# Optimization experiments

Hardware: AMD Instinct MI355X
Metric: run time of the kernel (lower is better)

Reference implementation:

```python
import jax, jax.numpy as jnp
import numpy as np

N, H, LAT, V = 256, 450, 56, 780  # nodes, hidden_size, latent_size, vocab_size


def _build_tree(seed=0):
    """Random tree on N nodes + DFS path matching the torch dfs() (children in ascending id order)."""
    rng = np.random.default_rng(seed)
    children = [[] for _ in range(N)]
    for i in range(1, N):
        children[int(rng.integers(0, i))].append(i)
    path = []
    stack = [(0, 0)]
    while stack:
        u, ci = stack.pop()
        ch = children[u]
        if ci < len(ch):
            stack.append((u, ci + 1))
            path.append((u, 1))   # descend to child -> stop flag 1
            stack.append((ch[ci], 0))
        else:
            path.append((u, 0))   # backtrack -> stop flag 0
    return path


def setup_inputs() -> dict:
    key = jax.random.key(0)
    ks = jax.random.split(key, 18)
    path = _build_tree()
    L = len(path)  # 2N-1 = 511
    node_ids = np.array([p[0] for p in path], dtype=np.int32)
    stops = np.array([p[1] for p in path], dtype=np.int32)
    next_ids = np.concatenate([node_ids[1:], np.zeros(1, np.int32)])
    label_steps = np.where(stops == 1)[0].astype(np.int32)  # N-1 steps that emit a label
    rng = np.random.default_rng(1)
    vids = rng.integers(0, V, size=N).astype(np.int32)
    node_feature = np.zeros((N, V), np.float32)
    node_feature[np.arange(N), vids] = 1.0  # one-hot vocab features, as in JT-VAE
    real_labels = np.concatenate([vids[:1], vids[next_ids[label_steps]]]).astype(np.int32)  # [N]
    w = lambda k, shape: (jax.random.normal(k, shape, jnp.float32) * 0.05)
    return {
        "latent_code": jax.random.normal(ks[0], (LAT,), jnp.float32),
        "node_feature": jnp.asarray(node_feature),
        "node_ids": jnp.asarray(node_ids),
        "next_ids": jnp.asarray(next_ids),
        "stops": jnp.asarray(stops),
        "label_steps": jnp.asarray(label_steps),
        "real_labels": jnp.asarray(real_labels),
        "Wz_w": w(ks[1], (H, V + H)), "Wz_b": w(ks[2], (H,)),
        "Ur_w": w(ks[3], (H, H)),
        "Wr_w": w(ks[4], (H, V)), "Wr_b": w(ks[5], (H,)),
        "Wh_w": w(ks[6], (H, V + H)), "Wh_b": w(ks[7], (H,)),
        "Wd12_w": w(ks[8], (H, V + LAT)), "Wd12_b": w(ks[9], (H,)),
        "Wd3_w": w(ks[10], (H, H)), "Wd3_b": w(ks[11], (H,)),
        "Ud_w": w(ks[12], (1, 2 * H)), "Ud_b": w(ks[13], (1,)),
        "Wl_w": w(ks[14], (H, H + LAT)), "Wl_b": w(ks[15], (H,)),
        "Ul_w": w(ks[16], (V, H)), "Ul_b": w(ks[17], (V,)),
    }


def reference(latent_code, node_feature, node_ids, next_ids, stops, label_steps, real_labels,
              Wz_w, Wz_b, Ur_w, Wr_w, Wr_b, Wh_w, Wh_b, Wd12_w, Wd12_b, Wd3_w, Wd3_b,
              Ud_w, Ud_b, Wl_w, Wl_b, Ul_w, Ul_b):
    n = node_feature.shape[0]
    h = Wz_w.shape[0]
    L = node_ids.shape[0]

    # Root label: F.relu(U_l(W_l(cat(latent, zeros(h)))))  -- relu OUTSIDE U_l, no softmax.
    root_in = jnp.concatenate([latent_code, jnp.zeros((h,), latent_code.dtype)])
    root_label = jax.nn.relu((root_in @ Wl_w.T + Wl_b) @ Ul_w.T + Ul_b)

    def step(carry, xs):
        hidden, enc = carry            # hidden: [n,n,h], enc: [n,n]
        a, b, is_last = xs
        x = node_feature[a]            # [V] one-hot row
        hs = hidden[:, a]              # [n,h] incoming messages into node a
        # Stop prediction (uses pre-update hidden)
        d12 = jnp.concatenate([x, latent_code]) @ Wd12_w.T + Wd12_b
        d3 = hs.sum(0) @ Wd3_w.T + Wd3_b
        pred_stop = (jax.nn.relu(jnp.concatenate([d12, d3])) @ Ud_w.T + Ud_b)[0]
        # GRU message a -> b, excluding the edge (a,b) from the neighbor mask
        enc0 = enc.at[a, b].set(0.0).at[b, a].set(0.0)
        mask = enc0[:, a]              # [n]
        Hm = hs * mask[:, None]        # masked gathered hidden
        s = Hm.sum(0)                  # [h]
        z = jax.nn.sigmoid(jnp.concatenate([x, s]) @ Wz_w.T + Wz_b)
        r1 = x @ Wr_w.T + Wr_b         # [h]
        r = jax.nn.sigmoid(r1 + Hm @ Ur_w.T)  # [n,h]; torch sums sigmoid over ALL n rows
        gated = jnp.tanh(jnp.concatenate([x, r.sum(0)]) @ Wh_w.T + Wh_b)
        new_h = (1.0 - z) * s + z * gated
        hidden_new = hidden.at[a, b].set(new_h)
        enc_new = enc0.at[a, b].set(1.0).at[b, a].set(1.0)
        hidden = jnp.where(is_last, hidden, hidden_new)  # last path entry: break before update
        enc = jnp.where(is_last, enc, enc_new)
        # Child label: softmax(U_l(relu(W_l(cat(latent, new_h)))))  -- relu INSIDE, then softmax
        lab_in = jnp.concatenate([latent_code, new_h])
        label = jax.nn.softmax(jax.nn.relu(lab_in @ Wl_w.T + Wl_b) @ Ul_w.T + Ul_b)
        return (hidden, enc), (pred_stop, label)

    hidden0 = jnp.zeros((n, n, h), jnp.float32)
    enc0 = jnp.zeros((n, n), jnp.float32)
    is_last = jnp.arange(L) == (L - 1)
    (_, _), (pred_stops, labels) = jax.lax.scan(step, (hidden0, enc0), (node_ids, next_ids, is_last))
    pred_labels = jnp.concatenate([root_label[None], labels[label_steps]], axis=0)  # [N, V]
    return stops.astype(jnp.float32), pred_stops, real_labels, pred_labels
```

## Files before the change

### kernel.cpp

```cpp
#include <hip/hip_runtime.h>
#include <math.h>

#define NN   256
#define HH   450
#define LATD 56
#define VV   780
#define LL   511
#define GSEQ 32
#define TSEQ 512
#define KMAX 15
#define AST  16

__device__ __forceinline__ float wred_sum(float v) {
    for (int off = 32; off; off >>= 1) v += __shfl_down(v, off, 64);
    return v;
}

__device__ __forceinline__ void axch64(unsigned long long* p, unsigned long long v) {
    (void)__hip_atomic_exchange(p, v, __ATOMIC_RELAXED, __HIP_MEMORY_SCOPE_AGENT);
}
__device__ __forceinline__ unsigned long long ardw64(unsigned long long* p) {
    return __hip_atomic_fetch_or(p, 0ull, __ATOMIC_RELAXED, __HIP_MEMORY_SCOPE_AGENT);
}
__device__ __forceinline__ unsigned long long pk64(float v, unsigned tag) {
    return ((unsigned long long)tag << 32) | (unsigned long long)__float_as_uint(v);
}
__device__ __forceinline__ float lo32f(unsigned long long x) { return __uint_as_float((unsigned)x); }
__device__ __forceinline__ unsigned hi32(unsigned long long x) { return (unsigned)(x >> 32); }

__global__ void k_vid(const float* __restrict__ nf, int* __restrict__ vid) {
    const int u = blockIdx.x;
    for (int v = threadIdx.x; v < VV; v += blockDim.x)
        if (nf[(size_t)u * VV + v] > 0.5f) vid[u] = v;
}

__global__ __launch_bounds__(512) void k_consts(
    const int* __restrict__ vid, const float* __restrict__ latent,
    const float* __restrict__ Wz, const float* __restrict__ Wzb,
    const float* __restrict__ Wr, const float* __restrict__ Wrb,
    const float* __restrict__ Wh, const float* __restrict__ Whb,
    const float* __restrict__ Wd12, const float* __restrict__ Wd12b,
    const float* __restrict__ Ud,
    float* __restrict__ cz, float* __restrict__ r1s, float* __restrict__ sig0,
    float* __restrict__ ch, float* __restrict__ dotd12)
{
    const int u = blockIdx.x, tid = threadIdx.x;
    const int v = vid[u];
    __shared__ float red[8];
    float p = 0.f;
    if (tid < HH) {
        const int i = tid, o = u * HH + i;
        cz[o] = Wz[(size_t)i * (VV + HH) + v] + Wzb[i];
        const float r1 = Wr[(size_t)i * VV + v] + Wrb[i];
        r1s[o] = r1;
        sig0[o] = 1.f / (1.f + expf(-r1));
        ch[o] = Wh[(size_t)i * (VV + HH) + v] + Whb[i];
        float d = Wd12[(size_t)i * (VV + LATD) + v] + Wd12b[i];
        for (int k = 0; k < LATD; ++k)
            d += Wd12[(size_t)i * (VV + LATD) + VV + k] * latent[k];
        p = Ud[i] * fmaxf(d, 0.f);
    }
    p = wred_sum(p);
    if ((tid & 63) == 0) red[tid >> 6] = p;
    __syncthreads();
    if (tid == 0) {
        float s = 0.f;
        for (int w = 0; w < 8; ++w) s += red[w];
        dotd12[u] = s;
    }
}

__global__ __launch_bounds__(512) void k_whsig0(
    const float* __restrict__ Wh, const float* __restrict__ sig0, float* __restrict__ out)
{
    const int u = blockIdx.x, tid = threadIdx.x, wave = tid >> 6, lane = tid & 63;
    __shared__ float sg[HH];
    if (tid < HH) sg[tid] = sig0[u * HH + tid];
    __syncthreads();
    for (int r = wave; r < HH; r += 8) {
        float acc = 0.f;
        for (int k = lane; k < HH; k += 64)
            acc += Wh[(size_t)r * (VV + HH) + VV + k] * sg[k];
        acc = wred_sum(acc);
        if (lane == 0) out[u * HH + r] = acc;
    }
}

__global__ void k_excl(const int* __restrict__ node_ids, const int* __restrict__ next_ids,
                       int* __restrict__ excl, float* __restrict__ ccpre)
{
    const int t = blockIdx.x;
    __shared__ int ex, cnt;
    if (threadIdx.x == 0) { ex = -1; cnt = 0; }
    __syncthreads();
    const int a = node_ids[t], b = next_ids[t];
    for (int tp = threadIdx.x; tp <= t; tp += blockDim.x) {
        if (tp < t && node_ids[tp] == b && next_ids[tp] == a) ex = tp;
        if (tp >= 1 && node_ids[tp] == a) atomicAdd(&cnt, 1);
    }
    __syncthreads();
    if (threadIdx.x == 0) {
        excl[t] = ex;
        ccpre[t] = 256.f - (float)cnt + (ex >= 0 ? 1.f : 0.f);
    }
}

__global__ void k_copy(const int* __restrict__ stops, const int* __restrict__ reall,
                       float* __restrict__ out)
{
    const int i = blockIdx.x * blockDim.x + threadIdx.x;
    if (i < LL) { out[i] = (float)stops[i]; out[LL + i] = 0.f; }
    if (i < NN) out[2 * LL + i] = (float)reall[i];
}

__global__ void k_pred(const float* __restrict__ pred_part, float* __restrict__ out) {
    const int t = blockIdx.x * blockDim.x + threadIdx.x;
    if (t < LL) {
        float s = 0.f;
        #pragma unroll 8
        for (int b = 0; b < GSEQ; ++b) s += pred_part[(size_t)t * GSEQ + b];
        out[LL + t] = s;
    }
}

#define KEEP16(w) asm volatile("" : \
    "+v"(w[0]), "+v"(w[1]), "+v"(w[2]),  "+v"(w[3]),  "+v"(w[4]),  "+v"(w[5]),  "+v"(w[6]),  "+v"(w[7]), \
    "+v"(w[8]), "+v"(w[9]), "+v"(w[10]), "+v"(w[11]), "+v"(w[12]), "+v"(w[13]), "+v"(w[14]), "+v"(w[15]))

__global__ __launch_bounds__(TSEQ, 2) void k_seq(
    const int* __restrict__ node_ids, const int* __restrict__ excl,
    const float* __restrict__ ccpre,
    const float* __restrict__ Ur, const float* __restrict__ Wz,
    const float* __restrict__ Wh, const float* __restrict__ Wd3,
    const float* __restrict__ Wd3b, const float* __restrict__ Ud,
    const float* __restrict__ Udb,
    const float* __restrict__ cz, const float* __restrict__ r1s,
    const float* __restrict__ ch, const float* __restrict__ WhSig0,
    const float* __restrict__ dotd12,
    float* __restrict__ Wd3SmL,
    float* __restrict__ NewHL, float* __restrict__ WzML, float* __restrict__ WhSvL,
    unsigned long long* __restrict__ bcNh, unsigned long long* __restrict__ bcSig,
    float* __restrict__ pred_part)
{
    const int tid = threadIdx.x, bid = blockIdx.x;
    const int wave = tid >> 6, lane = tid & 63;
    const int kcnt = 14 + (bid < 2 ? 1 : 0);
    const int kbeg = 14 * bid + (bid < 2 ? bid : 2);

    float* myWd3S = Wd3SmL + (size_t)bid * NN * AST;
    float* myNewH = NewHL  + (size_t)bid * LL * AST;
    float* myWzM  = WzML   + (size_t)bid * LL * AST;
    float* myWhSv = WhSvL  + (size_t)bid * LL * AST;

    __shared__ float sSm[NN * AST];
    __shared__ float sWzSm[NN * AST];
    __shared__ float sWhRs[NN * AST];
    __shared__ float nh_full[512];
    __shared__ float sig_full[512];
    __shared__ float sNhR[4][AST];
    __shared__ float sWzR[4][AST];
    __shared__ float sWhR[4][AST];

    float urw[16], wzw[16], wd3w[16], whw[16];
    #pragma unroll
    for (int it = 0; it < 2; ++it) {
        const int j = wave + 8 * it;
        const bool vj = j < kcnt;
        const int r = vj ? (kbeg + j) : 0;
        #pragma unroll
        for (int e = 0; e < 8; ++e) {
            const int c = lane + 64 * e;
            const bool vc = vj && (c < HH);
            urw[it * 8 + e]  = vc ? Ur[(size_t)r * HH + c] : 0.f;
            wzw[it * 8 + e]  = vc ? Wz[(size_t)r * (VV + HH) + VV + c] : 0.f;
            wd3w[it * 8 + e] = vc ? Wd3[(size_t)r * HH + c] : 0.f;
            whw[it * 8 + e]  = vc ? Wh[(size_t)r * (VV + HH) + VV + c] : 0.f;
        }
    }
    float ud_r = 0.f, w3b_r = 0.f;
    if (tid < kcnt) { ud_r = Ud[HH + kbeg + tid]; w3b_r = Wd3b[kbeg + tid]; }
    const float udb0 = Udb[0];

    for (int i = tid; i < NN * AST; i += TSEQ) { sSm[i] = 0.f; sWzSm[i] = 0.f; sWhRs[i] = 0.f; }
    nh_full[tid] = 0.f; sig_full[tid] = 0.f;

    int ap = node_ids[0];
    float pcz = 0.f, pch = 0.f, pws = 0.f;
    if (tid < kcnt) {
        const int o = ap * HH + kbeg + tid;
        pcz = cz[o]; pch = ch[o]; pws = WhSig0[o];
    }
    float pcc = ccpre[0];
    int  pidx = excl[0];
    float pe_nh = 0.f, pe_wz = 0.f, pe_wh = 0.f;
    __syncthreads();

    for (int t = 1; t <= LL; ++t) {
        KEEP16(urw); KEEP16(wzw); KEEP16(wd3w); KEEP16(whw);
        const int idx = pidx;
        float nh = 0.f;
        if (tid < kcnt) {
            const int oa = ap * AST + tid;
            float zarg = sWzSm[oa] + pcz;
            float whv  = sWhRs[oa] + pch;
            float sv   = sSm[oa];
            if (idx >= 0) {
                float enh, ewz, ewh;
                if (idx >= t - 4) {
                    const int sl = idx & 3;
                    enh = sNhR[sl][tid]; ewz = sWzR[sl][tid]; ewh = sWhR[sl][tid];
                } else {
                    enh = pe_nh; ewz = pe_wz; ewh = pe_wh;
                }
                zarg -= ewz; whv -= ewh; sv -= enh;
            }
            whv += pcc * pws;
            const float z = 1.f / (1.f + expf(-zarg));
            nh = (1.f - z) * sv + z * tanhf(whv);
            if (t < LL)
                axch64(&bcNh[(size_t)((t & 1) * 512 + kbeg + tid)], pk64(nh, (unsigned)t));
            myNewH[(t - 1) * AST + tid] = nh;
            sNhR[(t - 1) & 3][tid] = nh;
        }
        if (wave == 0) {
            float ps = 0.f;
            if (tid < kcnt)
                ps = ud_r * fmaxf(myWd3S[ap * AST + tid] + w3b_r, 0.f);
            ps = wred_sum(ps);
            if (lane == 0) {
                if (bid == 0) ps += dotd12[ap] + udb0;
                pred_part[(size_t)(t - 1) * GSEQ + bid] = ps;
            }
        }
        if (t == LL) break;
        const int a = node_ids[t];
        const unsigned tag = (unsigned)t;
        const int p = t & 1;

        pidx = excl[t];
        pe_nh = pe_wz = pe_wh = 0.f;
        if (pidx >= 0 && pidx < t - 3 && tid < kcnt) {
            const int oe = pidx * AST + tid;
            pe_nh = myNewH[oe]; pe_wz = myWzM[oe]; pe_wh = myWhSv[oe];
        }
        float r1v[2];
        #pragma unroll
        for (int it = 0; it < 2; ++it) {
            const int j = wave + 8 * it;
            r1v[it] = r1s[(size_t)a * HH + ((j < kcnt) ? (kbeg + j) : 0)];
        }
        if (tid < kcnt) sSm[a * AST + tid] += nh;

        if (tid < HH) {
            unsigned long long* pp = &bcNh[(size_t)(p * 512 + tid)];
            unsigned long long e = ardw64(pp);
            while (hi32(e) != tag) { __builtin_amdgcn_s_sleep(1); e = ardw64(pp); }
            nh_full[tid] = lo32f(e);
        }
        __syncthreads();

        #pragma unroll
        for (int it = 0; it < 2; ++it) {
            const int j = wave + 8 * it;
            float acc = 0.f;
            #pragma unroll
            for (int e = 0; e < 8; ++e) acc += urw[it * 8 + e] * nh_full[lane + 64 * e];
            acc = wred_sum(acc);
            if (lane == 0 && j < kcnt) {
                const float sg = 1.f / (1.f + expf(-(acc + r1v[it])));
                axch64(&bcSig[(size_t)(p * 512 + kbeg + j)], pk64(sg, tag));
            }
        }

        #pragma unroll
        for (int it = 0; it < 2; ++it) {
            const int j = wave + 8 * it;
            float az = 0.f, ad = 0.f;
            #pragma unroll
            for (int e = 0; e < 8; ++e) {
                const float x = nh_full[lane + 64 * e];
                az += wzw[it * 8 + e] * x;
                ad += wd3w[it * 8 + e] * x;
            }
            az = wred_sum(az); ad = wred_sum(ad);
            if (lane == 0 && j < kcnt) {
                myWzM[(t - 1) * AST + j] = az;
                sWzR[(t - 1) & 3][j] = az;
                sWzSm[a * AST + j] += az;
                myWd3S[a * AST + j] += ad;
            }
        }
        if (tid < kcnt) {
            const int o = a * HH + kbeg + tid;
            pcz = cz[o]; pch = ch[o]; pws = WhSig0[o];
        }
        pcc = ccpre[t];

        if (tid < HH) {
            unsigned long long* pp = &bcSig[(size_t)(p * 512 + tid)];
            unsigned long long e = ardw64(pp);
            while (hi32(e) != tag) { __builtin_amdgcn_s_sleep(1); e = ardw64(pp); }
            sig_full[tid] = lo32f(e);
        }
        __syncthreads();

        #pragma unroll
        for (int it = 0; it < 2; ++it) {
            const int j = wave + 8 * it;
            float aw = 0.f;
            #pragma unroll
            for (int e = 0; e < 8; ++e) aw += whw[it * 8 + e] * sig_full[lane + 64 * e];
            aw = wred_sum(aw);
            if (lane == 0 && j < kcnt) {
                myWhSv[(t - 1) * AST + j] = aw;
                sWhR[(t - 1) & 3][j] = aw;
                sWhRs[a * AST + j] += aw;
            }
        }
        ap = a;
        __syncthreads();
    }
}

__global__ __launch_bounds__(512) void k_label(
    const float* __restrict__ latent, const int* __restrict__ lsteps,
    const float* __restrict__ NewHL,
    const float* __restrict__ Wl, const float* __restrict__ Wlb,
    const float* __restrict__ Ul, const float* __restrict__ Ulb,
    float* __restrict__ out)
{
    const int q = blockIdx.x, tid = threadIdx.x, wave = tid >> 6, lane = tid & 63;
    __shared__ float inp[LATD + HH];
    __shared__ float t2[HH];
    __shared__ float lg[VV];
    __shared__ float red[8];
    if (tid < LATD) inp[tid] = latent[tid];
    if (q == 0) {
        if (tid < HH) inp[LATD + tid] = 0.f;
    } else {
        const int t = lsteps[q - 1];
        if (tid < HH) {
            const int b = (tid < 30) ? (tid / 15) : (2 + (tid - 30) / 14);
            const int j = (tid < 30) ? (tid % 15) : ((tid - 30) % 14);
            inp[LATD + tid] = NewHL[((size_t)b * LL + t) * AST + j];
        }
    }
    __syncthreads();
    for (int r = wave; r < HH; r += 8) {
        float acc = 0.f;
        for (int k = lane; k < LATD + HH; k += 64)
            acc += Wl[(size_t)r * (LATD + HH) + k] * inp[k];
        acc = wred_sum(acc);
        if (lane == 0) {
            const float v = acc + Wlb[r];
            t2[r] = (q == 0) ? v : fmaxf(v, 0.f);
        }
    }
    __syncthreads();
    for (int r = wave; r < VV; r += 8) {
        float acc = 0.f;
        for (int k = lane; k < HH; k += 64) acc += Ul[(size_t)r * HH + k] * t2[k];
        acc = wred_sum(acc);
        if (lane == 0) lg[r] = acc + Ulb[r];
    }
    __syncthreads();
    float* outrow = out + 2 * LL + NN + (size_t)q * VV;
    if (q == 0) {
        for (int i = tid; i < VV; i += 512) outrow[i] = fmaxf(lg[i], 0.f);
        return;
    }
    float mx = -1e30f;
    for (int i = tid; i < VV; i += 512) mx = fmaxf(mx, lg[i]);
    for (int off = 32; off; off >>= 1) mx = fmaxf(mx, __shfl_down(mx, off, 64));
    if (lane == 0) red[wave] = mx;
    __syncthreads();
    if (tid == 0) {
        float m = red[0];
        for (int w = 1; w < 8; ++w) m = fmaxf(m, red[w]);
        red[0] = m;
    }
    __syncthreads();
    const float M = red[0];
    float sum = 0.f;
    for (int i = tid; i < VV; i += 512) { const float e = expf(lg[i] - M); lg[i] = e; sum += e; }
    __syncthreads();
    sum = wred_sum(sum);
    if (lane == 0) red[wave] = sum;
    __syncthreads();
    if (tid == 0) {
        float s = 0.f;
        for (int w = 0; w < 8; ++w) s += red[w];
        red[0] = s;
    }
    __syncthreads();
    const float S = red[0];
    for (int i = tid; i < VV; i += 512) outrow[i] = lg[i] / S;
}

extern "C" void kernel_launch(void* const* d_in, const int* in_sizes, int n_in,
                              void* d_out, int out_size, void* d_ws, size_t ws_size,
                              hipStream_t stream)
{
    const float* latent = (const float*)d_in[0];
    const float* nodef  = (const float*)d_in[1];
    const int* node_ids = (const int*)d_in[2];
    const int* next_ids = (const int*)d_in[3];
    const int* stops    = (const int*)d_in[4];
    const int* lsteps   = (const int*)d_in[5];
    const int* reall    = (const int*)d_in[6];
    const float* Wz   = (const float*)d_in[7];
    const float* Wzb  = (const float*)d_in[8];
    const float* Urw  = (const float*)d_in[9];
    const float* Wr   = (const float*)d_in[10];
    const float* Wrb  = (const float*)d_in[11];
    const float* Wh   = (const float*)d_in[12];
    const float* Whb  = (const float*)d_in[13];
    const float* Wd12 = (const float*)d_in[14];
    const float* Wd12b= (const float*)d_in[15];
    const float* Wd3  = (const float*)d_in[16];
    const float* Wd3b = (const float*)d_in[17];
    const float* Ud   = (const float*)d_in[18];
    const float* Udb  = (const float*)d_in[19];
    const float* Wl   = (const float*)d_in[20];
    const float* Wlb  = (const float*)d_in[21];
    const float* Ul   = (const float*)d_in[22];
    const float* Ulb  = (const float*)d_in[23];
    (void)in_sizes; (void)n_in; (void)out_size; (void)ws_size;
    float* out = (float*)d_out;
    float* W = (float*)d_ws;

    size_t o = 0;
    float* Wd3SmL = W + o; o += (size_t)GSEQ * NN * AST;
    unsigned long long* bcNh  = (unsigned long long*)(W + o); o += 2 * 512 * 2;
    unsigned long long* bcSig = (unsigned long long*)(W + o); o += 2 * 512 * 2;
    const size_t zero_floats = o;
    int*   vid    = (int*)(W + o); o += NN;
    int*   excl   = (int*)(W + o); o += LL + 1;
    float* ccpre  = W + o; o += LL + 1;
    float* cz     = W + o; o += NN * HH;
    float* r1s    = W + o; o += NN * HH;
    float* sig0   = W + o; o += NN * HH;
    float* ch     = W + o; o += NN * HH;
    float* WhSig0 = W + o; o += NN * HH;
    float* dotd12 = W + o; o += NN;
    float* NewHL  = W + o; o += (size_t)GSEQ * LL * AST;
    float* WzML   = W + o; o += (size_t)GSEQ * LL * AST;
    float* WhSvL  = W + o; o += (size_t)GSEQ * LL * AST;
    float* predp  = W + o; o += (size_t)LL * GSEQ;

    hipMemsetAsync(W, 0, zero_floats * sizeof(float), stream);
    k_vid   <<<NN, 256, 0, stream>>>(nodef, vid);
    k_consts<<<NN, 512, 0, stream>>>(vid, latent, Wz, Wzb, Wr, Wrb, Wh, Whb,
                                     Wd12, Wd12b, Ud, cz, r1s, sig0, ch, dotd12);
    k_whsig0<<<NN, 512, 0, stream>>>(Wh, sig0, WhSig0);
    k_excl  <<<LL, 256, 0, stream>>>(node_ids, next_ids, excl, ccpre);
    k_copy  <<<2, 256, 0, stream>>>(stops, reall, out);
    k_seq   <<<GSEQ, TSEQ, 0, stream>>>(node_ids, excl, ccpre, Urw, Wz, Wh, Wd3, Wd3b,
                                        Ud, Udb, cz, r1s, ch, WhSig0, dotd12,
                                        Wd3SmL, NewHL, WzML, WhSvL,
                                        bcNh, bcSig,
                                        predp);
    k_pred  <<<1, 512, 0, stream>>>(predp, out);
    k_label <<<NN, 512, 0, stream>>>(latent, lsteps, NewHL, Wl, Wlb, Ul, Ulb, out);
}
```

Baseline: 2.579 ms.

## Streamline cross-block sequential sync: atomic loads, pipelined polling, LDS-resident accumulators

The cross-block broadcast now uses plain atomic stores and loads instead of exchange and fetch-or, and polling issues several loads in flight rather than sleeping between reads. Each block writes its own rows straight into LDS and skips polling them. Barriers wait only on LDS counters. The Wd3 accumulator moves from global memory into LDS, the exclusion ring grows from 4 to 8 entries, and next-step constants are prefetched earlier. The aim is to cut per-step latency in the 511-step serial loop. The costs are higher LDS use, occupancy limited to one block per CU, and busy-polling that adds memory traffic.

Result: faster. 2.283 ms (-11.5%).

```diff
diff --git a/kernel.cpp b/kernel.cpp
--- a/kernel.cpp
+++ b/kernel.cpp
@@ -10,23 +10,41 @@
 #define TSEQ 512
 #define KMAX 15
 #define AST  16
+#define RING 8
 
 __device__ __forceinline__ float wred_sum(float v) {
     for (int off = 32; off; off >>= 1) v += __shfl_down(v, off, 64);
     return v;
 }
 
-__device__ __forceinline__ void axch64(unsigned long long* p, unsigned long long v) {
-    (void)__hip_atomic_exchange(p, v, __ATOMIC_RELAXED, __HIP_MEMORY_SCOPE_AGENT);
-}
-__device__ __forceinline__ unsigned long long ardw64(unsigned long long* p) {
-    return __hip_atomic_fetch_or(p, 0ull, __ATOMIC_RELAXED, __HIP_MEMORY_SCOPE_AGENT);
+__device__ __forceinline__ void barrier_lds() {
+    asm volatile("s_waitcnt lgkmcnt(0)" ::: "memory");
+    __builtin_amdgcn_s_barrier();
+}
+
+__device__ __forceinline__ void ast64(unsigned long long* p, unsigned long long v) {
+    __hip_atomic_store(p, v, __ATOMIC_RELAXED, __HIP_MEMORY_SCOPE_AGENT);
+}
+__device__ __forceinline__ unsigned long long ald64(const unsigned long long* p) {
+    return __hip_atomic_load(p, __ATOMIC_RELAXED, __HIP_MEMORY_SCOPE_AGENT);
 }
 __device__ __forceinline__ unsigned long long pk64(float v, unsigned tag) {
     return ((unsigned long long)tag << 32) | (unsigned long long)__float_as_uint(v);
 }
 __device__ __forceinline__ float lo32f(unsigned long long x) { return __uint_as_float((unsigned)x); }
 __device__ __forceinline__ unsigned hi32(unsigned long long x) { return (unsigned)(x >> 32); }
+
+__device__ __forceinline__ float poll4(const unsigned long long* pp, unsigned tag) {
+    unsigned long long a = ald64(pp);
+    if (hi32(a) == tag) return lo32f(a);
+    unsigned long long b = ald64(pp);
+    unsigned long long c = ald64(pp);
+    unsigned long long d = ald64(pp);
+    for (;;) {
+        if (hi32(a) == tag) return lo32f(a);
+        a = b; b = c; c = d; d = ald64(pp);
+    }
+}
 
 __global__ void k_vid(const float* __restrict__ nf, int* __restrict__ vid) {
     const int u = blockIdx.x;
@@ -127,7 +145,7 @@
     "+v"(w[0]), "+v"(w[1]), "+v"(w[2]),  "+v"(w[3]),  "+v"(w[4]),  "+v"(w[5]),  "+v"(w[6]),  "+v"(w[7]), \
     "+v"(w[8]), "+v"(w[9]), "+v"(w[10]), "+v"(w[11]), "+v"(w[12]), "+v"(w[13]), "+v"(w[14]), "+v"(w[15]))
 
-__global__ __launch_bounds__(TSEQ, 2) void k_seq(
+__global__ __launch_bounds__(TSEQ, 1) void k_seq(
     const int* __restrict__ node_ids, const int* __restrict__ excl,
     const float* __restrict__ ccpre,
     const float* __restrict__ Ur, const float* __restrict__ Wz,
@@ -137,7 +155,6 @@
     const float* __restrict__ cz, const float* __restrict__ r1s,
     const float* __restrict__ ch, const float* __restrict__ WhSig0,
     const float* __restrict__ dotd12,
-    float* __restrict__ Wd3SmL,
     float* __restrict__ NewHL, float* __restrict__ WzML, float* __restrict__ WhSvL,
     unsigned long long* __restrict__ bcNh, unsigned long long* __restrict__ bcSig,
     float* __restrict__ pred_part)
@@ -147,7 +164,6 @@
     const int kcnt = 14 + (bid < 2 ? 1 : 0);
     const int kbeg = 14 * bid + (bid < 2 ? bid : 2);
 
-    float* myWd3S = Wd3SmL + (size_t)bid * NN * AST;
     float* myNewH = NewHL  + (size_t)bid * LL * AST;
     float* myWzM  = WzML   + (size_t)bid * LL * AST;
     float* myWhSv = WhSvL  + (size_t)bid * LL * AST;
@@ -155,11 +171,12 @@
     __shared__ float sSm[NN * AST];
     __shared__ float sWzSm[NN * AST];
     __shared__ float sWhRs[NN * AST];
+    __shared__ float sWd3S[NN * AST];
     __shared__ float nh_full[512];
     __shared__ float sig_full[512];
-    __shared__ float sNhR[4][AST];
-    __shared__ float sWzR[4][AST];
-    __shared__ float sWhR[4][AST];
+    __shared__ float sNhR[RING][AST];
+    __shared__ float sWzR[RING][AST];
+    __shared__ float sWhR[RING][AST];
 
     float urw[16], wzw[16], wd3w[16], whw[16];
     #pragma unroll
@@ -177,11 +194,15 @@
             whw[it * 8 + e]  = vc ? Wh[(size_t)r * (VV + HH) + VV + c] : 0.f;
         }
     }
+    KEEP16(urw); KEEP16(wzw); KEEP16(wd3w); KEEP16(whw);
+
     float ud_r = 0.f, w3b_r = 0.f;
     if (tid < kcnt) { ud_r = Ud[HH + kbeg + tid]; w3b_r = Wd3b[kbeg + tid]; }
     const float udb0 = Udb[0];
 
-    for (int i = tid; i < NN * AST; i += TSEQ) { sSm[i] = 0.f; sWzSm[i] = 0.f; sWhRs[i] = 0.f; }
+    for (int i = tid; i < NN * AST; i += TSEQ) {
+        sSm[i] = 0.f; sWzSm[i] = 0.f; sWhRs[i] = 0.f; sWd3S[i] = 0.f;
+    }
     nh_full[tid] = 0.f; sig_full[tid] = 0.f;
 
     int ap = node_ids[0];
@@ -193,10 +214,10 @@
     float pcc = ccpre[0];
     int  pidx = excl[0];
     float pe_nh = 0.f, pe_wz = 0.f, pe_wh = 0.f;
+    const bool own_row = tid >= kbeg && tid < kbeg + kcnt;
     __syncthreads();
 
     for (int t = 1; t <= LL; ++t) {
-        KEEP16(urw); KEEP16(wzw); KEEP16(wd3w); KEEP16(whw);
         const int idx = pidx;
         float nh = 0.f;
         if (tid < kcnt) {
@@ -206,8 +227,8 @@
             float sv   = sSm[oa];
             if (idx >= 0) {
                 float enh, ewz, ewh;
-                if (idx >= t - 4) {
-                    const int sl = idx & 3;
+                if (idx >= t - RING) {
+                    const int sl = idx & (RING - 1);
                     enh = sNhR[sl][tid]; ewz = sWzR[sl][tid]; ewh = sWhR[sl][tid];
                 } else {
                     enh = pe_nh; ewz = pe_wz; ewh = pe_wh;
@@ -217,15 +238,17 @@
             whv += pcc * pws;
             const float z = 1.f / (1.f + expf(-zarg));
             nh = (1.f - z) * sv + z * tanhf(whv);
-            if (t < LL)
-                axch64(&bcNh[(size_t)((t & 1) * 512 + kbeg + tid)], pk64(nh, (unsigned)t));
+            if (t < LL) {
+                ast64(&bcNh[(size_t)((t & 1) * 512 + kbeg + tid)], pk64(nh, (unsigned)t));
+                nh_full[kbeg + tid] = nh;
+            }
             myNewH[(t - 1) * AST + tid] = nh;
-            sNhR[(t - 1) & 3][tid] = nh;
+            sNhR[(t - 1) & (RING - 1)][tid] = nh;
         }
         if (wave == 0) {
             float ps = 0.f;
             if (tid < kcnt)
-                ps = ud_r * fmaxf(myWd3S[ap * AST + tid] + w3b_r, 0.f);
+                ps = ud_r * fmaxf(sWd3S[ap * AST + tid] + w3b_r, 0.f);
             ps = wred_sum(ps);
             if (lane == 0) {
                 if (bid == 0) ps += dotd12[ap] + udb0;
@@ -239,7 +262,7 @@
 
         pidx = excl[t];
         pe_nh = pe_wz = pe_wh = 0.f;
-        if (pidx >= 0 && pidx < t - 3 && tid < kcnt) {
+        if (pidx >= 0 && pidx < t - (RING - 1) && tid < kcnt) {
             const int oe = pidx * AST + tid;
             pe_nh = myNewH[oe]; pe_wz = myWzM[oe]; pe_wh = myWhSv[oe];
         }
@@ -249,15 +272,17 @@
             const int j = wave + 8 * it;
             r1v[it] = r1s[(size_t)a * HH + ((j < kcnt) ? (kbeg + j) : 0)];
         }
+        float ncz = 0.f, nch = 0.f, nws = 0.f;
+        if (tid < kcnt) {
+            const int o = a * HH + kbeg + tid;
+            ncz = cz[o]; nch = ch[o]; nws = WhSig0[o];
+        }
+        const float ncc = ccpre[t];
         if (tid < kcnt) sSm[a * AST + tid] += nh;
 
-        if (tid < HH) {
-            unsigned long long* pp = &bcNh[(size_t)(p * 512 + tid)];
-            unsigned long long e = ardw64(pp);
-            while (hi32(e) != tag) { __builtin_amdgcn_s_sleep(1); e = ardw64(pp); }
-            nh_full[tid] = lo32f(e);
-        }
-        __syncthreads();
+        if (tid < HH && !own_row)
+            nh_full[tid] = poll4(&bcNh[(size_t)(p * 512 + tid)], tag);
+        barrier_lds();
 
         #pragma unroll
         for (int it = 0; it < 2; ++it) {
@@ -268,7 +293,8 @@
             acc = wred_sum(acc);
             if (lane == 0 && j < kcnt) {
                 const float sg = 1.f / (1.f + expf(-(acc + r1v[it])));
-                axch64(&bcSig[(size_t)(p * 512 + kbeg + j)], pk64(sg, tag));
+                ast64(&bcSig[(size_t)(p * 512 + kbeg + j)], pk64(sg, tag));
+                sig_full[kbeg + j] = sg;
             }
         }
 
@@ -285,24 +311,16 @@
             az = wred_sum(az); ad = wred_sum(ad);
             if (lane == 0 && j < kcnt) {
                 myWzM[(t - 1) * AST + j] = az;
-                sWzR[(t - 1) & 3][j] = az;
+                sWzR[(t - 1) & (RING - 1)][j] = az;
                 sWzSm[a * AST + j] += az;
-                myWd3S[a * AST + j] += ad;
-            }
-        }
-        if (tid < kcnt) {
-            const int o = a * HH + kbeg + tid;
-            pcz = cz[o]; pch = ch[o]; pws = WhSig0[o];
-        }
-        pcc = ccpre[t];
-
-        if (tid < HH) {
-            unsigned long long* pp = &bcSig[(size_t)(p * 512 + tid)];
-            unsigned long long e = ardw64(pp);
-            while (hi32(e) != tag) { __builtin_amdgcn_s_sleep(1); e = ardw64(pp); }
-            sig_full[tid] = lo32f(e);
-        }
-        __syncthreads();
+                sWd3S[a * AST + j] += ad;
+            }
+        }
+        pcz = ncz; pch = nch; pws = nws; pcc = ncc;
+
+        if (tid < HH && !own_row)
+            sig_full[tid] = poll4(&bcSig[(size_t)(p * 512 + tid)], tag);
+        barrier_lds();
 
         #pragma unroll
         for (int it = 0; it < 2; ++it) {
@@ -313,12 +331,12 @@
             aw = wred_sum(aw);
             if (lane == 0 && j < kcnt) {
                 myWhSv[(t - 1) * AST + j] = aw;
-                sWhR[(t - 1) & 3][j] = aw;
+                sWhR[(t - 1) & (RING - 1)][j] = aw;
                 sWhRs[a * AST + j] += aw;
             }
         }
         ap = a;
-        __syncthreads();
+        barrier_lds();
     }
 }
 
@@ -430,7 +448,6 @@
     float* W = (float*)d_ws;
 
     size_t o = 0;
-    float* Wd3SmL = W + o; o += (size_t)GSEQ * NN * AST;
     unsigned long long* bcNh  = (unsigned long long*)(W + o); o += 2 * 512 * 2;
     unsigned long long* bcSig = (unsigned long long*)(W + o); o += 2 * 512 * 2;
     const size_t zero_floats = o;
@@ -457,7 +474,7 @@
     k_copy  <<<2, 256, 0, stream>>>(stops, reall, out);
     k_seq   <<<GSEQ, TSEQ, 0, stream>>>(node_ids, excl, ccpre, Urw, Wz, Wh, Wd3, Wd3b,
                                         Ud, Udb, cz, r1s, ch, WhSig0, dotd12,
-                                        Wd3SmL, NewHL, WzML, WhSvL,
+                                        NewHL, WzML, WhSvL,
                                         bcNh, bcSig,
                                         predp);
     k_pred  <<<1, 512, 0, stream>>>(predp, out);
```
